# Kernel tuning notes

Hardware: AMD Instinct MI355X
Metric: run time of the kernel (lower is better)

## Reference

```python
import jax, jax.numpy as jnp
import numpy as np

B, T, IN, H, OUT = 1024, 512, 16, 64, 8


def setup_inputs() -> dict:
    key = jax.random.key(0)
    ks = jax.random.split(key, 7)
    s = 1.0 / np.sqrt(H)
    return {
        "x": jax.random.normal(ks[0], (B, T, IN), dtype=jnp.float32),
        "W_ih": jax.random.normal(ks[1], (4 * H, IN), dtype=jnp.float32) * s,
        "W_hh": jax.random.normal(ks[2], (4 * H, H), dtype=jnp.float32) * s,
        "b_ih": jax.random.normal(ks[3], (4 * H,), dtype=jnp.float32) * s,
        "b_hh": jax.random.normal(ks[4], (4 * H,), dtype=jnp.float32) * s,
        "W_fc": jax.random.normal(ks[5], (OUT, H), dtype=jnp.float32) * s,
        "b_fc": jax.random.normal(ks[6], (OUT,), dtype=jnp.float32) * s,
    }


def reference(x, W_ih, W_hh, b_ih, b_hh, W_fc, b_fc):
    Bq, Tq, _ = x.shape
    Hq = W_hh.shape[1]
    # Precompute input contribution for all timesteps: [T, B, 4H]
    xw = jnp.einsum("bti,gi->tbg", x, W_ih) + b_ih + b_hh

    def step(carry, xw_t):
        h, c = carry
        gates = xw_t + h @ W_hh.T  # [B, 4H]
        i, f, g, o = jnp.split(gates, 4, axis=-1)  # PyTorch gate order i,f,g,o
        i = jax.nn.sigmoid(i)
        f = jax.nn.sigmoid(f)
        g = jnp.tanh(g)
        o = jax.nn.sigmoid(o)
        c = f * c + i * g
        h = o * jnp.tanh(c)
        return (h, c), None

    h0 = jnp.zeros((Bq, Hq), dtype=x.dtype)
    c0 = jnp.zeros((Bq, Hq), dtype=x.dtype)
    (h_last, _), _ = jax.lax.scan(step, (h0, c0), xw)

    # fc on last timestep only, then sigmoid -> [B, 1, OUT]
    out = jax.nn.sigmoid(h_last @ W_fc.T + b_fc)
    return out[:, None, :]
```

## Files before the change

### kernel.cpp

```cpp
#include <hip/hip_runtime.h>
#include <math.h>


#define LSTM_T 512
#define LSTM_IN 16
#define LSTM_H 64
#define LSTM_OUT 8
#define BT 2
#define HSTRIDE 72

#define L2E   1.44269504088896340736f
#define L2E2  2.88539008177792681472f

typedef _Float16 half8  __attribute__((ext_vector_type(8)));
typedef float    floatx4 __attribute__((ext_vector_type(4)));

static __device__ __forceinline__ float fast_rcp(float x) { return __builtin_amdgcn_rcpf(x); }
static __device__ __forceinline__ float fast_exp2(float x) { return __builtin_amdgcn_exp2f(x); }
static __device__ __forceinline__ float sigm2(float p) { return fast_rcp(1.0f + fast_exp2(-p)); }
static __device__ __forceinline__ float tanh2(float p) {
    return fmaf(-2.0f, fast_rcp(1.0f + fast_exp2(p)), 1.0f);
}
static __device__ __forceinline__ void pin4(int4& v) {
    asm volatile("" : "+v"(v.x), "+v"(v.y), "+v"(v.z), "+v"(v.w));
}
static __device__ __forceinline__ void pinf4(float4& v) {
    asm volatile("" : "+v"(v.x), "+v"(v.y), "+v"(v.z), "+v"(v.w));
}
static __device__ __forceinline__ void lite_barrier() {
    asm volatile("s_waitcnt lgkmcnt(0)\n\ts_barrier" ::: "memory");
}
static __device__ __forceinline__ unsigned pk2h(float a, float b) {
    return __builtin_bit_cast(unsigned, __builtin_amdgcn_cvt_pkrtz(a, b));
}
static __device__ __forceinline__ half8 to_h8(float4 a, float4 b) {
    uint4 u = make_uint4(pk2h(a.x, a.y), pk2h(a.z, a.w), pk2h(b.x, b.y), pk2h(b.z, b.w));
    return __builtin_bit_cast(half8, u);
}
static __device__ __forceinline__ int4 cvt8h(float4 a, float4 b) {
    return __builtin_bit_cast(int4, to_h8(a, b));
}
static __device__ __forceinline__ float4 ld4(const float* p) {
    return *reinterpret_cast<const float4*>(p);
}
static __device__ __forceinline__ float sel4(floatx4 v, bool r0, bool r1) {
    float lo = r0 ? v[1] : v[0];
    float hi = r0 ? v[3] : v[2];
    return r1 ? hi : lo;
}
static __device__ __forceinline__ float swz8(float v) {
    int r = __builtin_amdgcn_ds_swizzle(__builtin_bit_cast(int, v), 0x201F);
    return __builtin_bit_cast(float, r);
}

__global__ __launch_bounds__(256, 2)
void lstm_mfma_kernel(const float* __restrict__ x,
                      const float* __restrict__ W_ih,
                      const float* __restrict__ W_hh,
                      const float* __restrict__ b_ih,
                      const float* __restrict__ b_hh,
                      const float* __restrict__ W_fc,
                      const float* __restrict__ b_fc,
                      float* __restrict__ out) {
    const int tid   = threadIdx.x;
    const int lane  = tid & 63;
    const int w     = tid >> 6;
    const int q     = lane >> 4;
    const int m     = lane & 15;
    const int b     = m & 1;
    const int rho   = (m >> 1) & 3;
    const bool r0   = (rho & 1) != 0;
    const bool r1   = (rho & 2) != 0;
    const bool h1   = (m & 8) != 0;
    const int jmine = 16 * w + 4 * q + rho;
    const bool wr   = (m < 8);
    const int bbase = blockIdx.x * BT;

    const float s1 = h1 ? L2E2 : -L2E;
    const float a1 = h1 ? 1.0f : 0.0f;
    const float b1 = h1 ? -2.0f : 1.0f;

    __shared__ __align__(16) _Float16 hbuf[2][BT][HSTRIDE];
    __shared__ __align__(16) float hfin[BT][LSTM_H];

    int4 Ah[4][2], Ax[4];
    float4 bias4[4];
    #pragma unroll
    for (int tt = 0; tt < 4; ++tt) {
        const int gt = tt * 64 + 16 * w + m;
        #pragma unroll
        for (int c = 0; c < 2; ++c) {
            const float* s = W_hh + gt * LSTM_H + 32 * c + 8 * q;
            Ah[tt][c] = cvt8h(ld4(s), ld4(s + 4));
            pin4(Ah[tt][c]);
        }
        float4 xa = make_float4(0.f, 0.f, 0.f, 0.f), xb = xa;
        if (q < 2) {
            const float* s = W_ih + gt * LSTM_IN + 8 * q;
            xa = ld4(s); xb = ld4(s + 4);
        }
        Ax[tt] = cvt8h(xa, xb);
        pin4(Ax[tt]);
        const int gb = tt * 64 + 16 * w + 4 * q;
        float4 bi = ld4(b_ih + gb), bh = ld4(b_hh + gb);
        bias4[tt] = make_float4(bi.x + bh.x, bi.y + bh.y, bi.z + bh.z, bi.w + bh.w);
        pinf4(bias4[tt]);
    }

    if (tid < 64) {
        int bb = tid >> 5, jj = tid & 31;
        reinterpret_cast<int*>(&hbuf[0][bb][0])[jj] = 0;
    }

    const float* xp = x + (size_t)(bbase + b) * LSTM_T * LSTM_IN + 8 * q;
    float4 xA0 = make_float4(0.f, 0.f, 0.f, 0.f), xA1 = xA0;
    float4 xB0 = xA0, xB1 = xA0;
    if (q < 2) {
        xA0 = ld4(xp);              xA1 = ld4(xp + 4);
        xB0 = ld4(xp + LSTM_IN);    xB1 = ld4(xp + LSTM_IN + 4);
    }
    __syncthreads();

    float creg = 0.0f, hreg = 0.0f;

#define STEP(T_, X0, X1)                                                        \
    {                                                                           \
        const _Float16* cur = &hbuf[(T_) & 1][0][0];                            \
        _Float16*       nxt = &hbuf[((T_) + 1) & 1][0][0];                      \
         \
        half8 bh0 = *reinterpret_cast<const half8*>(cur + b * HSTRIDE + 8 * q); \
        half8 bh1 = *reinterpret_cast<const half8*>(cur + b * HSTRIDE + 32 + 8 * q); \
        half8 xf = to_h8(X0, X1);                                               \
        floatx4 acc[4];                                                         \
        _Pragma("unroll")                                                       \
        for (int tt = 0; tt < 4; ++tt)                                          \
            acc[tt] = __builtin_amdgcn_mfma_f32_16x16x32_f16(                   \
                __builtin_bit_cast(half8, Ax[tt]), xf,                          \
                __builtin_bit_cast(floatx4, bias4[tt]), 0, 0, 0);               \
                       \
        if (q < 2 && (T_) + 2 < LSTM_T) {                                       \
            X0 = ld4(xp + (size_t)((T_) + 2) * LSTM_IN);                        \
            X1 = ld4(xp + (size_t)((T_) + 2) * LSTM_IN + 4);                    \
        }                                                                       \
        _Pragma("unroll")                                                       \
        for (int tt = 0; tt < 4; ++tt)                                          \
            acc[tt] = __builtin_amdgcn_mfma_f32_16x16x32_f16(                   \
                __builtin_bit_cast(half8, Ah[tt][0]), bh0, acc[tt], 0, 0, 0);   \
        _Pragma("unroll")                                                       \
        for (int tt = 0; tt < 4; ++tt)                                          \
            acc[tt] = __builtin_amdgcn_mfma_f32_16x16x32_f16(                   \
                __builtin_bit_cast(half8, Ah[tt][1]), bh1, acc[tt], 0, 0, 0);   \
               \
        floatx4 v1, v2;                                                         \
        _Pragma("unroll")                                                       \
        for (int r = 0; r < 4; ++r) {                                           \
            v1[r] = h1 ? acc[2][r] : acc[1][r];                                 \
            v2[r] = h1 ? acc[3][r] : acc[0][r];                                 \
        }                                                                       \
        float u1 = sel4(v1, r0, r1);                                            \
        float u2 = sel4(v2, r0, r1);                                            \
             \
        float act1 = fmaf(b1, fast_rcp(1.0f + fast_exp2(s1 * u1)), a1);         \
        float act2 = fast_rcp(1.0f + fast_exp2(-L2E * u2));   \
                \
        float g_in = swz8(act1);                                                \
        float o_in = swz8(act2);                                                \
            \
        creg = fmaf(act1, creg, act2 * g_in);                  \
        hreg = o_in * tanh2(creg * L2E2);                      \
        if (wr) nxt[b * HSTRIDE + jmine] = (_Float16)hreg;                      \
        lite_barrier();                                                         \
    }

    for (int t = 0; t < LSTM_T; t += 2) {
        STEP(t,     xA0, xA1)
        STEP(t + 1, xB0, xB1)
    }
#undef STEP

    if (wr) hfin[b][jmine] = hreg;
    __syncthreads();

    if (tid < BT * LSTM_OUT) {
        int bb = tid >> 3, o = tid & 7;
        float s = b_fc[o];
        #pragma unroll
        for (int j4 = 0; j4 < LSTM_H / 4; ++j4) {
            float4 wv = ld4(W_fc + o * LSTM_H + 4 * j4);
            float4 hv = *reinterpret_cast<const float4*>(&hfin[bb][4 * j4]);
            s = fmaf(wv.x, hv.x, s);
            s = fmaf(wv.y, hv.y, s);
            s = fmaf(wv.z, hv.z, s);
            s = fmaf(wv.w, hv.w, s);
        }
        out[(size_t)(bbase + bb) * LSTM_OUT + o] = sigm2(s * L2E);
    }
}

extern "C" void kernel_launch(void* const* d_in, const int* in_sizes, int n_in,
                              void* d_out, int out_size, void* d_ws, size_t ws_size,
                              hipStream_t stream) {
    const float* x    = (const float*)d_in[0];
    const float* W_ih = (const float*)d_in[1];
    const float* W_hh = (const float*)d_in[2];
    const float* b_ih = (const float*)d_in[3];
    const float* b_hh = (const float*)d_in[4];
    const float* W_fc = (const float*)d_in[5];
    const float* b_fc = (const float*)d_in[6];
    float* out = (float*)d_out;

    lstm_mfma_kernel<<<1024 / BT, 256, 0, stream>>>(
        x, W_ih, W_hh, b_ih, b_hh, W_fc, b_fc, out);
}
```

Baseline: 259.4 us.

## Fold activation scales into weights, use DPP shuffle and raise priority

Pre-scales the W_hh, W_ih and bias values per gate by -log2e or 2log2e so the exp2 arguments come straight out of the MFMA with no extra multiply. The cell state is kept pre-scaled by 2log2e. The ds_swizzle cross-lane exchange is replaced by a DPP row_shr update, which avoids the LDS-path latency. The activation section is wrapped in s_setprio, and all lanes now store unconditionally into a padded h buffer at an offset so the store branch disappears. The risks are fp16 rounding of the scaled weights and a DPP lane pattern that must match the swizzle it replaces.

```diff
diff --git a/kernel.cpp b/kernel.cpp
--- a/kernel.cpp
+++ b/kernel.cpp
@@ -7,7 +7,7 @@
 #define LSTM_H 64
 #define LSTM_OUT 8
 #define BT 2
-#define HSTRIDE 72
+#define HSTRIDE 136
 
 #define L2E   1.44269504088896340736f
 #define L2E2  2.88539008177792681472f
@@ -18,9 +18,6 @@
 static __device__ __forceinline__ float fast_rcp(float x) { return __builtin_amdgcn_rcpf(x); }
 static __device__ __forceinline__ float fast_exp2(float x) { return __builtin_amdgcn_exp2f(x); }
 static __device__ __forceinline__ float sigm2(float p) { return fast_rcp(1.0f + fast_exp2(-p)); }
-static __device__ __forceinline__ float tanh2(float p) {
-    return fmaf(-2.0f, fast_rcp(1.0f + fast_exp2(p)), 1.0f);
-}
 static __device__ __forceinline__ void pin4(int4& v) {
     asm volatile("" : "+v"(v.x), "+v"(v.y), "+v"(v.z), "+v"(v.w));
 }
@@ -42,14 +39,18 @@
 }
 static __device__ __forceinline__ float4 ld4(const float* p) {
     return *reinterpret_cast<const float4*>(p);
+}
+static __device__ __forceinline__ float4 scl4(float4 v, float s) {
+    return make_float4(s * v.x, s * v.y, s * v.z, s * v.w);
 }
 static __device__ __forceinline__ float sel4(floatx4 v, bool r0, bool r1) {
     float lo = r0 ? v[1] : v[0];
     float hi = r0 ? v[3] : v[2];
     return r1 ? hi : lo;
 }
-static __device__ __forceinline__ float swz8(float v) {
-    int r = __builtin_amdgcn_ds_swizzle(__builtin_bit_cast(int, v), 0x201F);
+static __device__ __forceinline__ float dpp8(float v) {
+    int r = __builtin_amdgcn_update_dpp(0, __builtin_bit_cast(int, v),
+                                        0x128, 0xF, 0xF, false);
     return __builtin_bit_cast(float, r);
 }
 
@@ -74,9 +75,9 @@
     const bool h1   = (m & 8) != 0;
     const int jmine = 16 * w + 4 * q + rho;
     const bool wr   = (m < 8);
+    const int woff  = b * HSTRIDE + jmine + (h1 ? 64 : 0);
     const int bbase = blockIdx.x * BT;
 
-    const float s1 = h1 ? L2E2 : -L2E;
     const float a1 = h1 ? 1.0f : 0.0f;
     const float b1 = h1 ? -2.0f : 1.0f;
 
@@ -87,11 +88,12 @@
     float4 bias4[4];
     #pragma unroll
     for (int tt = 0; tt < 4; ++tt) {
+        const float sc = (tt == 2) ? L2E2 : -L2E;
         const int gt = tt * 64 + 16 * w + m;
         #pragma unroll
         for (int c = 0; c < 2; ++c) {
             const float* s = W_hh + gt * LSTM_H + 32 * c + 8 * q;
-            Ah[tt][c] = cvt8h(ld4(s), ld4(s + 4));
+            Ah[tt][c] = cvt8h(scl4(ld4(s), sc), scl4(ld4(s + 4), sc));
             pin4(Ah[tt][c]);
         }
         float4 xa = make_float4(0.f, 0.f, 0.f, 0.f), xb = xa;
@@ -99,11 +101,12 @@
             const float* s = W_ih + gt * LSTM_IN + 8 * q;
             xa = ld4(s); xb = ld4(s + 4);
         }
-        Ax[tt] = cvt8h(xa, xb);
+        Ax[tt] = cvt8h(scl4(xa, sc), scl4(xb, sc));
         pin4(Ax[tt]);
         const int gb = tt * 64 + 16 * w + 4 * q;
         float4 bi = ld4(b_ih + gb), bh = ld4(b_hh + gb);
-        bias4[tt] = make_float4(bi.x + bh.x, bi.y + bh.y, bi.z + bh.z, bi.w + bh.w);
+        bias4[tt] = make_float4(sc * (bi.x + bh.x), sc * (bi.y + bh.y),
+                                sc * (bi.z + bh.z), sc * (bi.w + bh.w));
         pinf4(bias4[tt]);
     }
 
@@ -121,7 +124,7 @@
     }
     __syncthreads();
 
-    float creg = 0.0f, hreg = 0.0f;
+    float cs = 0.0f, hreg = 0.0f;
 
 #define STEP(T_, X0, X1)                                                        \
     {                                                                           \
@@ -150,6 +153,7 @@
         for (int tt = 0; tt < 4; ++tt)                                          \
             acc[tt] = __builtin_amdgcn_mfma_f32_16x16x32_f16(                   \
                 __builtin_bit_cast(half8, Ah[tt][1]), bh1, acc[tt], 0, 0, 0);   \
+        __builtin_amdgcn_s_setprio(1);                                          \
                \
         floatx4 v1, v2;                                                         \
         _Pragma("unroll")                                                       \
@@ -159,16 +163,20 @@
         }                                                                       \
         float u1 = sel4(v1, r0, r1);                                            \
         float u2 = sel4(v2, r0, r1);                                            \
-             \
-        float act1 = fmaf(b1, fast_rcp(1.0f + fast_exp2(s1 * u1)), a1);         \
-        float act2 = fast_rcp(1.0f + fast_exp2(-L2E * u2));   \
-                \
-        float g_in = swz8(act1);                                                \
-        float o_in = swz8(act2);                                                \
+                  \
+        float act1 = fmaf(b1, fast_rcp(1.0f + fast_exp2(u1)), a1);              \
+        float act2 = fast_rcp(1.0f + fast_exp2(u2));          \
+        float act2K = act2 * L2E2;                   \
             \
-        creg = fmaf(act1, creg, act2 * g_in);                  \
-        hreg = o_in * tanh2(creg * L2E2);                      \
-        if (wr) nxt[b * HSTRIDE + jmine] = (_Float16)hreg;                      \
+        float g_in = dpp8(act1);                                                \
+        float o_in = dpp8(act2);                                                \
+        \
+        cs = fmaf(act1, cs, act2K * g_in);                                      \
+        float th = fmaf(-2.0f, fast_rcp(1.0f + fast_exp2(cs)), 1.0f);           \
+        hreg = o_in * th;                                                       \
+                   \
+        nxt[woff] = (_Float16)hreg;                                             \
+        __builtin_amdgcn_s_setprio(0);                                          \
         lite_barrier();                                                         \
     }
 
```

New measurement: 251.4 us. 1.03x faster.
